# Performance work log

Hardware: AMD Instinct MI355X
Metric: run time of the kernel (lower is better)

The kernel has to match this reference:

```python
import jax, jax.numpy as jnp
import numpy as np

N, E, D, DE, H = 50000, 400000, 128, 64, 8
EPS = 1e-5
SLOPE = 0.2


def setup_inputs() -> dict:
    key = jax.random.key(0)
    ks = jax.random.split(key, 16)

    def lin(k, fan_in, fan_out):
        return (jax.random.normal(k, (fan_in, fan_out), jnp.float32) / np.sqrt(fan_in)).astype(jnp.float32)

    return {
        "node_features": jax.random.normal(ks[0], (N, D), jnp.float32),
        "edge_features": jax.random.normal(ks[1], (E, DE), jnp.float32),
        "Wn": lin(ks[2], D, D), "bn": jnp.zeros((D,), jnp.float32),
        "Wq": lin(ks[3], D, D), "bq": jnp.zeros((D,), jnp.float32),
        "Wk": lin(ks[4], D, D), "bk": jnp.zeros((D,), jnp.float32),
        "Wv": lin(ks[5], D, D), "bv": jnp.zeros((D,), jnp.float32),
        "We": lin(ks[6], DE, D), "be": jnp.zeros((D,), jnp.float32),
        "A1": lin(ks[7], 3 * D, D), "b1": jnp.zeros((D,), jnp.float32),
        "A2": lin(ks[8], D, H), "b2": jnp.zeros((H,), jnp.float32),
        "gamma": jnp.ones((D,), jnp.float32),
        "beta": jnp.zeros((D,), jnp.float32),
        "edge_index": jax.random.randint(ks[9], (2, E), 0, N, dtype=jnp.int32),
    }


def reference(node_features, edge_features, Wn, bn, Wq, bq, Wk, bk, Wv, bv,
              We, be, A1, b1, A2, b2, gamma, beta, edge_index):
    num_nodes = node_features.shape[0]
    h = node_features @ Wn + bn                      # [N, D]
    q = node_features @ Wq + bq                      # [N, D]
    k = node_features @ Wk + bk                      # [N, D]
    v = node_features @ Wv + bv                      # [N, D]
    eh = edge_features @ We + be                     # [E, D]

    src, tgt = edge_index[0], edge_index[1]
    attn_in = jnp.concatenate([q[src], k[tgt], eh], axis=-1)   # [E, 3D]
    hmid = jax.nn.leaky_relu(attn_in @ A1 + b1, SLOPE)          # [E, D]
    scores = jax.nn.leaky_relu(hmid @ A2 + b2, SLOPE)           # [E, H]
    w = jax.nn.softmax(scores.mean(axis=-1), axis=0)            # global softmax over edges, [E]

    # scatter-add: output[src] += w * v[tgt]
    out = jax.ops.segment_sum(w[:, None] * v[tgt], src, num_segments=num_nodes)  # [N, D]

    y = h + out                                       # dropout = identity (eval)
    mu = y.mean(axis=-1, keepdims=True)
    var = y.var(axis=-1, keepdims=True)
    return gamma * (y - mu) / jnp.sqrt(var + EPS) + beta
```

## Files before the change

### kernel.cpp

```cpp
#include <hip/hip_runtime.h>

#define D 128
#define DE 64
#define SLOPE 0.2f
#define EPS 1e-5f

typedef float f32x4 __attribute__((ext_vector_type(4)));
typedef short bf16x8 __attribute__((ext_vector_type(8)));
typedef unsigned short ushort;

__device__ __forceinline__ float lrelu(float x) { return x > 0.f ? x : SLOPE * x; }

__device__ __forceinline__ ushort f2bf(float x) {
  union { float f; unsigned u; } c; c.f = x;
  unsigned r = c.u + 0x7FFFu + ((c.u >> 16) & 1u);
  return (ushort)(r >> 16);
}
__device__ __forceinline__ float bf2f(unsigned u) {
  return __uint_as_float(u << 16);
}
__device__ __forceinline__ uint4 cvt8(const float* p) {
  float4 f0 = *(const float4*)p;
  float4 f1 = *(const float4*)(p + 4);
  union { ushort us[8]; uint4 v; } u;
  u.us[0] = f2bf(f0.x); u.us[1] = f2bf(f0.y);
  u.us[2] = f2bf(f0.z); u.us[3] = f2bf(f0.w);
  u.us[4] = f2bf(f1.x); u.us[5] = f2bf(f1.y);
  u.us[6] = f2bf(f1.z); u.us[7] = f2bf(f1.w);
  return u.v;
}

__global__ __launch_bounds__(128) void fold_pack(
    const float* __restrict__ Wq, const float* __restrict__ Wk,
    const float* __restrict__ We, const float* __restrict__ A1,
    const float* __restrict__ bq, const float* __restrict__ bk,
    const float* __restrict__ be, const float* __restrict__ b1,
    const float* __restrict__ Wn, const float* __restrict__ Wv,
    ushort* __restrict__ AfqP, ushort* __restrict__ AfkP,
    ushort* __restrict__ AfeT, float* __restrict__ bfold,
    ushort* __restrict__ WnP, ushort* __restrict__ WvP,
    const int* __restrict__ src, int* __restrict__ deg, int E) {
  int r = blockIdx.x;
  int j = threadIdx.x;
  if (r < 128) {
    float acc = 0.f;
    for (int t = 0; t < 128; ++t) acc += Wq[r * 128 + t] * A1[t * 128 + j];
    int ch = r >> 5, quad = (r >> 3) & 3, jj = r & 7, nt = j >> 4, l15 = j & 15;
    AfqP[(((ch * 8 + nt) * 4 + quad) * 16 + l15) * 8 + jj] = f2bf(acc);
  } else if (r < 256) {
    int k = r - 128;
    float acc = 0.f;
    for (int t = 0; t < 128; ++t) acc += Wk[k * 128 + t] * A1[(128 + t) * 128 + j];
    int ch = k >> 5, quad = (k >> 3) & 3, jj = k & 7, nt = j >> 4, l15 = j & 15;
    AfkP[(((ch * 8 + nt) * 4 + quad) * 16 + l15) * 8 + jj] = f2bf(acc);
  } else if (r < 320) {
    int k = r - 256;
    float acc = 0.f;
    for (int t = 0; t < 128; ++t) acc += We[k * 128 + t] * A1[(256 + t) * 128 + j];
    AfeT[j * 64 + k] = f2bf(acc);
  } else if (r == 320) {
    float acc = b1[j];
    for (int t = 0; t < 128; ++t) {
      acc += bq[t] * A1[t * 128 + j];
      acc += bk[t] * A1[(128 + t) * 128 + j];
      acc += be[t] * A1[(256 + t) * 128 + j];
    }
    bfold[j] = acc;
  } else if (r < 449) {
    int c = r - 321;
    int ch = j >> 5, quad = (j >> 3) & 3, jj = j & 7, nt = c >> 4, l15 = c & 15;
    WnP[(((ch * 8 + nt) * 4 + quad) * 16 + l15) * 8 + jj] = f2bf(Wn[j * 128 + c]);
  } else if (r < 577) {
    int c = r - 449;
    int ch = j >> 5, quad = (j >> 3) & 3, jj = j & 7, nt = c >> 4, l15 = c & 15;
    WvP[(((ch * 8 + nt) * 4 + quad) * 16 + l15) * 8 + jj] = f2bf(Wv[j * 128 + c]);
  } else {
    int i = (r - 577) * 128 + j;
    if (i < E) atomicAdd(&deg[src[i]], 1);
  }
}

__global__ __launch_bounds__(256, 2) void node_gemm_mfma(
    const float* __restrict__ X, const ushort* __restrict__ WnP,
    const ushort* __restrict__ WvP, const ushort* __restrict__ AfqP,
    const ushort* __restrict__ AfkP, const float* __restrict__ bn,
    const float* __restrict__ bv, float* __restrict__ h,
    ushort* __restrict__ vb, ushort* __restrict__ q2p,
    ushort* __restrict__ k2p, int Nn) {
  __shared__ ushort As[128 * 40];
  __shared__ float bS[128];
  const ushort* BP;
  const float* bb = nullptr;
  float* O = nullptr;
  ushort* Ob = nullptr;
  int mode;
  switch (blockIdx.y) {
    case 0: BP = WnP; bb = bn; O = h; mode = 0; break;
    case 1: BP = WvP; bb = bv; Ob = vb; mode = 1; break;
    case 2: BP = AfqP; Ob = q2p; mode = 2; break;
    default: BP = AfkP; Ob = k2p; mode = 2; break;
  }
  const int t = threadIdx.x;
  if (t < 128) bS[t] = bb ? bb[t] : 0.f;
  const int seg = t & 3, arow = t >> 2;
  const int m0 = blockIdx.x * 128;
  int rIdx[2];
#pragma unroll
  for (int l = 0; l < 2; ++l) rIdx[l] = min(m0 + arow + 64 * l, Nn - 1);
  uint4 avA[2];
#pragma unroll
  for (int l = 0; l < 2; ++l)
    avA[l] = cvt8(X + (size_t)rIdx[l] * 128 + seg * 8);
  f32x4 acc[2][8];
#pragma unroll
  for (int mt = 0; mt < 2; ++mt)
#pragma unroll
    for (int nt = 0; nt < 8; ++nt) acc[mt][nt] = (f32x4)(0.f);
  const int lane = t & 63, wv = t >> 6, l15 = lane & 15, quad = lane >> 4;
  for (int ch = 0; ch < 4; ++ch) {
#pragma unroll
    for (int l = 0; l < 2; ++l)
      *(uint4*)&As[(arow + 64 * l) * 40 + seg * 8] = avA[l];
    __syncthreads();
    if (ch < 3) {
      int o = (ch + 1) * 32 + seg * 8;
#pragma unroll
      for (int l = 0; l < 2; ++l)
        avA[l] = cvt8(X + (size_t)rIdx[l] * 128 + o);
    }
    bf16x8 af[2];
#pragma unroll
    for (int mt = 0; mt < 2; ++mt)
      af[mt] = *(const bf16x8*)&As[(wv * 32 + mt * 16 + l15) * 40 + quad * 8];
    const ushort* bp = BP + ((size_t)(ch * 8) * 64 + lane) * 8;
#pragma unroll
    for (int nt = 0; nt < 8; ++nt) {
      bf16x8 bfr = *(const bf16x8*)(bp + nt * 512);
#pragma unroll
      for (int mt = 0; mt < 2; ++mt)
        acc[mt][nt] =
            __builtin_amdgcn_mfma_f32_16x16x32_bf16(af[mt], bfr, acc[mt][nt], 0, 0, 0);
    }
    __syncthreads();
  }
#pragma unroll
  for (int mt = 0; mt < 2; ++mt) {
    int rowb = m0 + wv * 32 + mt * 16 + quad * 4;
#pragma unroll
    for (int nt = 0; nt < 8; ++nt) {
      int col = nt * 16 + l15;
      float b = bS[col];
#pragma unroll
      for (int r = 0; r < 4; ++r) {
        int rg = rowb + r;
        if (rg < Nn) {
          if (mode == 0)      O[(size_t)rg * 128 + col] = acc[mt][nt][r] + b;
          else if (mode == 1) Ob[(size_t)rg * 128 + col] = f2bf(acc[mt][nt][r] + b);
          else                Ob[(size_t)rg * 128 + l15 * 8 + nt] = f2bf(acc[mt][nt][r]);
        }
      }
    }
  }
}

__global__ __launch_bounds__(256, 3) void edge_fused4(
    const float* __restrict__ EF, const ushort* __restrict__ AfeT,
    const float* __restrict__ bfold, const float* __restrict__ A2,
    const float* __restrict__ b2, const ushort* __restrict__ q2p,
    const ushort* __restrict__ k2p, const int* __restrict__ src,
    const int* __restrict__ tgt, int* __restrict__ cursor,
    int2* __restrict__ cwt, float2* __restrict__ part, int E) {
  __shared__ ushort As[128 * 40];
  __shared__ ushort Bs[128 * 40];
  __shared__ float A2s[128 * 9];
  __shared__ float bfS[128];
  __shared__ float b2s[8];
  __shared__ int sIdxS[128], sIdxT[128];
  __shared__ float redM[16], redS[16];
  const int t = threadIdx.x;
  const int e0 = blockIdx.x * 128;
  if (t < 128) {
    sIdxS[t] = src[min(e0 + t, E - 1)];
    bfS[t] = bfold[t];
  } else {
    sIdxT[t - 128] = tgt[min(e0 + t - 128, E - 1)];
  }
  if (t < 8) b2s[t] = b2[t];
#pragma unroll
  for (int l = 0; l < 4; ++l) {
    int i = t + l * 256;
    A2s[(i >> 3) * 9 + (i & 7)] = A2[i];
  }
  const int seg = t & 3, arow = t >> 2;
  int ecl[2];
#pragma unroll
  for (int l = 0; l < 2; ++l) ecl[l] = min(e0 + arow + 64 * l, E - 1);
  uint4 avA[2], avB[2];
#pragma unroll
  for (int l = 0; l < 2; ++l) {
    avA[l] = cvt8(EF + (size_t)ecl[l] * 64 + seg * 8);
    avB[l] = *(const uint4*)(AfeT + (arow + 64 * l) * 64 + seg * 8);
  }
  f32x4 acc[2][8];
#pragma unroll
  for (int mt = 0; mt < 2; ++mt)
#pragma unroll
    for (int nt = 0; nt < 8; ++nt) acc[mt][nt] = (f32x4)(0.f);
  const int lane = t & 63, wv = t >> 6, l15 = lane & 15, quad = lane >> 4;

#pragma unroll
  for (int ch = 0; ch < 2; ++ch) {
#pragma unroll
    for (int l = 0; l < 2; ++l) {
      *(uint4*)&As[(arow + 64 * l) * 40 + seg * 8] = avA[l];
      *(uint4*)&Bs[(arow + 64 * l) * 40 + seg * 8] = avB[l];
    }
    __syncthreads();
    if (ch == 0) {
      int o = 32 + seg * 8;
#pragma unroll
      for (int l = 0; l < 2; ++l) {
        avA[l] = cvt8(EF + (size_t)ecl[l] * 64 + o);
        avB[l] = *(const uint4*)(AfeT + (arow + 64 * l) * 64 + o);
      }
    }
    bf16x8 af[2];
#pragma unroll
    for (int mt = 0; mt < 2; ++mt)
      af[mt] = *(const bf16x8*)&As[(wv * 32 + mt * 16 + l15) * 40 + quad * 8];
#pragma unroll
    for (int nt = 0; nt < 8; ++nt) {
      bf16x8 bfr = *(const bf16x8*)&Bs[(nt * 16 + l15) * 40 + quad * 8];
#pragma unroll
      for (int mt = 0; mt < 2; ++mt)
        acc[mt][nt] =
            __builtin_amdgcn_mfma_f32_16x16x32_bf16(af[mt], bfr, acc[mt][nt], 0, 0, 0);
    }
    if (ch == 0) __syncthreads();
  }

  float bfv[8];
#pragma unroll
  for (int nt = 0; nt < 8; ++nt) bfv[nt] = bfS[nt * 16 + l15];
#pragma unroll
  for (int mt = 0; mt < 2; ++mt) {
#pragma unroll
    for (int r = 0; r < 4; ++r) {
      int erow = wv * 32 + mt * 16 + quad * 4 + r;
      int si = sIdxS[erow], ti = sIdxT[erow];
      uint4 qv = *(const uint4*)(q2p + (size_t)si * 128 + l15 * 8);
      uint4 kv = *(const uint4*)(k2p + (size_t)ti * 128 + l15 * 8);
      const ushort* qs = (const ushort*)&qv;
      const ushort* ks = (const ushort*)&kv;
#pragma unroll
      for (int nt = 0; nt < 8; ++nt)
        acc[mt][nt][r] =
            lrelu(acc[mt][nt][r] + bf2f(qs[nt]) + bf2f(ks[nt]) + bfv[nt]);
    }
  }
  float tacc[2][4];
#pragma unroll
  for (int mt = 0; mt < 2; ++mt)
#pragma unroll
    for (int r = 0; r < 4; ++r) tacc[mt][r] = 0.f;
  for (int hh = 0; hh < 8; ++hh) {
    float a2v[8];
#pragma unroll
    for (int nt = 0; nt < 8; ++nt) a2v[nt] = A2s[nt * 144 + l15 * 9 + hh];
    float b2h = b2s[hh];
#pragma unroll
    for (int mt = 0; mt < 2; ++mt)
#pragma unroll
      for (int r = 0; r < 4; ++r) {
        float p = 0.f;
#pragma unroll
        for (int nt = 0; nt < 8; ++nt) p += acc[mt][nt][r] * a2v[nt];
        p += __shfl_xor(p, 1);
        p += __shfl_xor(p, 2);
        p += __shfl_xor(p, 4);
        p += __shfl_xor(p, 8);
        tacc[mt][r] += lrelu(p + b2h);
      }
  }
  if (l15 == 0) {
    float sc[8];
    float m = -1e30f;
#pragma unroll
    for (int mt = 0; mt < 2; ++mt)
#pragma unroll
      for (int r = 0; r < 4; ++r) {
        int i = mt * 4 + r;
        sc[i] = tacc[mt][r] * 0.125f;
        int e = e0 + wv * 32 + mt * 16 + quad * 4 + r;
        if (e < E) m = fmaxf(m, sc[i]);
      }
    float ssum = 0.f;
#pragma unroll
    for (int mt = 0; mt < 2; ++mt)
#pragma unroll
      for (int r = 0; r < 4; ++r) {
        int i = mt * 4 + r;
        int erow = wv * 32 + mt * 16 + quad * 4 + r;
        if (e0 + erow < E) {
          ssum += __expf(sc[i] - m);
          int j = atomicAdd(&cursor[sIdxS[erow]], 1);
          cwt[j] = make_int2(sIdxT[erow], __float_as_int(sc[i]));
        }
      }
    int rid = wv * 4 + quad;
    redM[rid] = m;
    redS[rid] = ssum;
  }
  __syncthreads();
  if (t == 0) {
    float M = redM[0], S = redS[0];
#pragma unroll
    for (int i = 1; i < 16; ++i) {
      float m2 = redM[i], s2 = redS[i];
      float Mn = fmaxf(M, m2);
      S = S * __expf(M - Mn) + s2 * __expf(m2 - Mn);
      M = Mn;
    }
    part[blockIdx.x] = make_float2(M, S);
  }
}

__global__ __launch_bounds__(256) void softmax_final(
    const float2* __restrict__ part, int nPart, float* __restrict__ MS) {
  __shared__ float mS[256], sS[256];
  int tid = threadIdx.x;
  float m = -1e30f, sum = 0.f;
  for (int i = tid; i < nPart; i += 256) {
    float2 p = part[i];
    float M = fmaxf(m, p.x);
    sum = sum * __expf(m - M) + p.y * __expf(p.x - M);
    m = M;
  }
  mS[tid] = m;
  sS[tid] = sum;
  __syncthreads();
  for (int off = 128; off > 0; off >>= 1) {
    if (tid < off) {
      float m1 = mS[tid], s1 = sS[tid];
      float m2 = mS[tid + off], s2 = sS[tid + off];
      float M = fmaxf(m1, m2);
      mS[tid] = M;
      sS[tid] = s1 * __expf(m1 - M) + s2 * __expf(m2 - M);
    }
    __syncthreads();
  }
  if (tid == 0) {
    MS[0] = mS[0];
    MS[1] = 1.f / sS[0];
  }
}

__global__ __launch_bounds__(256) void scan1(const int* __restrict__ deg,
                                             int* __restrict__ incl,
                                             int* __restrict__ bsum, int N) {
  __shared__ int sh[256];
  int tid = threadIdx.x;
  int i = blockIdx.x * 256 + tid;
  sh[tid] = (i < N) ? deg[i] : 0;
  __syncthreads();
  for (int off = 1; off < 256; off <<= 1) {
    int tv = (tid >= off) ? sh[tid - off] : 0;
    __syncthreads();
    sh[tid] += tv;
    __syncthreads();
  }
  if (i < N) incl[i] = sh[tid];
  if (tid == 255) bsum[blockIdx.x] = sh[255];
}

__global__ __launch_bounds__(256) void scan2(int* __restrict__ bsum, int nb) {
  __shared__ int sh[256];
  int tid = threadIdx.x;
  sh[tid] = (tid < nb) ? bsum[tid] : 0;
  __syncthreads();
  for (int off = 1; off < 256; off <<= 1) {
    int tv = (tid >= off) ? sh[tid - off] : 0;
    __syncthreads();
    sh[tid] += tv;
    __syncthreads();
  }
  if (tid < nb) bsum[tid] = sh[tid];
}

__global__ __launch_bounds__(256) void scan3(const int* __restrict__ deg,
                                             const int* __restrict__ incl,
                                             const int* __restrict__ bsum,
                                             int* __restrict__ offs,
                                             int* __restrict__ cursor, int N,
                                             int E) {
  int i = blockIdx.x * 256 + threadIdx.x;
  if (i >= N) return;
  int base = (blockIdx.x > 0) ? bsum[blockIdx.x - 1] : 0;
  int ex = incl[i] - deg[i] + base;
  offs[i] = ex;
  cursor[i] = ex;
  if (i == N - 1) offs[N] = E;
}

__global__ __launch_bounds__(256) void gather_ln(
    const int* __restrict__ offs, const int2* __restrict__ cwt,
    const ushort* __restrict__ vb, const float* __restrict__ MS,
    const float* __restrict__ gamma, const float* __restrict__ beta,
    float* __restrict__ y, int N) {
  int tid = threadIdx.x;
  int n = blockIdx.x * 4 + (tid >> 6);
  if (n >= N) return;
  int lane = tid & 63;
  float M = MS[0], inv = MS[1];
  int beg = offs[n], end = offs[n + 1];
  float a0 = 0.f, a1 = 0.f;
  int j = beg;
  for (; j + 4 <= end; j += 4) {
    int2 p0 = cwt[j], p1 = cwt[j + 1], p2 = cwt[j + 2], p3 = cwt[j + 3];
    unsigned u0 = *(const unsigned*)(vb + (size_t)p0.x * 128 + lane * 2);
    unsigned u1 = *(const unsigned*)(vb + (size_t)p1.x * 128 + lane * 2);
    unsigned u2 = *(const unsigned*)(vb + (size_t)p2.x * 128 + lane * 2);
    unsigned u3 = *(const unsigned*)(vb + (size_t)p3.x * 128 + lane * 2);
    float w0 = __expf(__int_as_float(p0.y) - M) * inv;
    float w1 = __expf(__int_as_float(p1.y) - M) * inv;
    float w2 = __expf(__int_as_float(p2.y) - M) * inv;
    float w3 = __expf(__int_as_float(p3.y) - M) * inv;
    a0 += w0 * bf2f(u0 & 0xffffu) + w1 * bf2f(u1 & 0xffffu) +
          w2 * bf2f(u2 & 0xffffu) + w3 * bf2f(u3 & 0xffffu);
    a1 += w0 * bf2f(u0 >> 16) + w1 * bf2f(u1 >> 16) + w2 * bf2f(u2 >> 16) +
          w3 * bf2f(u3 >> 16);
  }
  for (; j < end; ++j) {
    int2 p = cwt[j];
    float w = __expf(__int_as_float(p.y) - M) * inv;
    unsigned u = *(const unsigned*)(vb + (size_t)p.x * 128 + lane * 2);
    a0 += w * bf2f(u & 0xffffu);
    a1 += w * bf2f(u >> 16);
  }
  size_t base = (size_t)n * 128 + lane * 2;
  float2 hv = *(const float2*)(y + base);
  float y0 = hv.x + a0, y1 = hv.y + a1;
  float sum = y0 + y1, ssq = y0 * y0 + y1 * y1;
#pragma unroll
  for (int off = 1; off < 64; off <<= 1) {
    sum += __shfl_xor(sum, off);
    ssq += __shfl_xor(ssq, off);
  }
  float mu = sum * (1.f / 128.f);
  float var = ssq * (1.f / 128.f) - mu * mu;
  float rstd = rsqrtf(var + EPS);
  float2 g = *(const float2*)(gamma + lane * 2);
  float2 bt = *(const float2*)(beta + lane * 2);
  float2 out;
  out.x = g.x * (y0 - mu) * rstd + bt.x;
  out.y = g.y * (y1 - mu) * rstd + bt.y;
  *(float2*)(y + base) = out;
}

extern "C" void kernel_launch(void* const* d_in, const int* in_sizes, int n_in,
                              void* d_out, int out_size, void* d_ws,
                              size_t ws_size, hipStream_t stream) {
  const float* X  = (const float*)d_in[0];
  const float* EF = (const float*)d_in[1];
  const float* Wn = (const float*)d_in[2];
  const float* bn = (const float*)d_in[3];
  const float* Wq = (const float*)d_in[4];
  const float* bq = (const float*)d_in[5];
  const float* Wk = (const float*)d_in[6];
  const float* bk = (const float*)d_in[7];
  const float* Wv = (const float*)d_in[8];
  const float* bv = (const float*)d_in[9];
  const float* We = (const float*)d_in[10];
  const float* be = (const float*)d_in[11];
  const float* A1 = (const float*)d_in[12];
  const float* b1 = (const float*)d_in[13];
  const float* A2 = (const float*)d_in[14];
  const float* b2 = (const float*)d_in[15];
  const float* gamma = (const float*)d_in[16];
  const float* beta  = (const float*)d_in[17];
  const int* ei = (const int*)d_in[18];

  int N = in_sizes[0] / D;
  int E = in_sizes[1] / DE;
  const int* src = ei;
  const int* tgt = ei + E;

  float* h = (float*)d_out;
  float* ws = (float*)d_ws;
  float2* part = (float2*)ws;
  float* MS    = (float*)(part + 4096);
  float* bfold = MS + 4;
  ushort* vb   = (ushort*)(bfold + 128);
  ushort* q2p  = vb + (size_t)N * D;
  ushort* k2p  = q2p + (size_t)N * D;
  ushort* AfqP = k2p + (size_t)N * D;
  ushort* AfkP = AfqP + 128 * 128;
  ushort* AfeT = AfkP + 128 * 128;
  ushort* WnP  = AfeT + 128 * 64;
  ushort* WvP  = WnP + 128 * 128;
  int* deg    = (int*)(WvP + 128 * 128);
  int* incl   = deg + N;
  int* bsum   = incl + N;
  int* cursor = bsum + 256;
  int* offs   = cursor + N;
  int2* cwt   = (int2*)(offs + N + 2);

  int nbScan = (N + 255) / 256;
  int nbEdge = (E + 127) / 128;
  int nbHist = (E + 127) / 128;

  hipMemsetAsync(deg, 0, (size_t)N * sizeof(int), stream);
  fold_pack<<<577 + nbHist, 128, 0, stream>>>(Wq, Wk, We, A1, bq, bk, be, b1,
                                              Wn, Wv, AfqP, AfkP, AfeT, bfold,
                                              WnP, WvP, src, deg, E);
  scan1<<<nbScan, 256, 0, stream>>>(deg, incl, bsum, N);
  scan2<<<1, 256, 0, stream>>>(bsum, nbScan);
  scan3<<<nbScan, 256, 0, stream>>>(deg, incl, bsum, offs, cursor, N, E);
  node_gemm_mfma<<<dim3((N + 127) / 128, 4), 256, 0, stream>>>(
      X, WnP, WvP, AfqP, AfkP, bn, bv, h, vb, q2p, k2p, N);
  edge_fused4<<<nbEdge, 256, 0, stream>>>(EF, AfeT, bfold, A2, b2, q2p, k2p,
                                          src, tgt, cursor, cwt, part, E);
  softmax_final<<<1, 256, 0, stream>>>(part, nbEdge, MS);
  gather_ln<<<(N + 3) / 4, 256, 0, stream>>>(offs, cwt, vb, MS, gamma, beta, h,
                                             N);
}
```

Measured before the change: 381.1 us.

## Fuse four node GEMMs into one kernel sharing a staged input tile

The node GEMM previously ran four grid slices (Wn, Wv, folded q, folded k), each reloading and converting the same 128-row block of node features from global memory. Now each block stages its full 128x128 bf16 input tile into shared memory once and loops over the four weight sets, reusing the tile. This cuts X reads and conversions fourfold. In exchange the grid has a quarter as many blocks, shared memory per block grows to about 35 KB, and the chunked prefetch overlap of the old loop is gone.

```diff
diff --git a/kernel.cpp b/kernel.cpp
--- a/kernel.cpp
+++ b/kernel.cpp
@@ -80,83 +80,81 @@
   }
 }
 
-__global__ __launch_bounds__(256, 2) void node_gemm_mfma(
+__global__ __launch_bounds__(256, 2) void node_gemm_fused(
     const float* __restrict__ X, const ushort* __restrict__ WnP,
     const ushort* __restrict__ WvP, const ushort* __restrict__ AfqP,
     const ushort* __restrict__ AfkP, const float* __restrict__ bn,
     const float* __restrict__ bv, float* __restrict__ h,
     ushort* __restrict__ vb, ushort* __restrict__ q2p,
     ushort* __restrict__ k2p, int Nn) {
-  __shared__ ushort As[128 * 40];
-  __shared__ float bS[128];
-  const ushort* BP;
-  const float* bb = nullptr;
-  float* O = nullptr;
-  ushort* Ob = nullptr;
-  int mode;
-  switch (blockIdx.y) {
-    case 0: BP = WnP; bb = bn; O = h; mode = 0; break;
-    case 1: BP = WvP; bb = bv; Ob = vb; mode = 1; break;
-    case 2: BP = AfqP; Ob = q2p; mode = 2; break;
-    default: BP = AfkP; Ob = k2p; mode = 2; break;
-  }
+  __shared__ ushort As[128 * 136];
+  __shared__ float bnS[128], bvS[128];
   const int t = threadIdx.x;
-  if (t < 128) bS[t] = bb ? bb[t] : 0.f;
-  const int seg = t & 3, arow = t >> 2;
+  if (t < 128) {
+    bnS[t] = bn[t];
+    bvS[t] = bv[t];
+  }
   const int m0 = blockIdx.x * 128;
-  int rIdx[2];
-#pragma unroll
-  for (int l = 0; l < 2; ++l) rIdx[l] = min(m0 + arow + 64 * l, Nn - 1);
-  uint4 avA[2];
-#pragma unroll
-  for (int l = 0; l < 2; ++l)
-    avA[l] = cvt8(X + (size_t)rIdx[l] * 128 + seg * 8);
-  f32x4 acc[2][8];
-#pragma unroll
-  for (int mt = 0; mt < 2; ++mt)
-#pragma unroll
-    for (int nt = 0; nt < 8; ++nt) acc[mt][nt] = (f32x4)(0.f);
+  {
+    int row = t >> 1, half = t & 1;
+    int rg = min(m0 + row, Nn - 1);
+    const float* xp = X + (size_t)rg * 128 + half * 64;
+    ushort* ap = &As[row * 136 + half * 64];
+#pragma unroll
+    for (int s = 0; s < 8; ++s) *(uint4*)(ap + s * 8) = cvt8(xp + s * 8);
+  }
+  __syncthreads();
   const int lane = t & 63, wv = t >> 6, l15 = lane & 15, quad = lane >> 4;
-  for (int ch = 0; ch < 4; ++ch) {
-#pragma unroll
-    for (int l = 0; l < 2; ++l)
-      *(uint4*)&As[(arow + 64 * l) * 40 + seg * 8] = avA[l];
-    __syncthreads();
-    if (ch < 3) {
-      int o = (ch + 1) * 32 + seg * 8;
-#pragma unroll
-      for (int l = 0; l < 2; ++l)
-        avA[l] = cvt8(X + (size_t)rIdx[l] * 128 + o);
-    }
-    bf16x8 af[2];
+#pragma unroll 1
+  for (int mode = 0; mode < 4; ++mode) {
+    const ushort* BP;
+    switch (mode) {
+      case 0: BP = WnP; break;
+      case 1: BP = WvP; break;
+      case 2: BP = AfqP; break;
+      default: BP = AfkP; break;
+    }
+    f32x4 acc[2][8];
 #pragma unroll
     for (int mt = 0; mt < 2; ++mt)
-      af[mt] = *(const bf16x8*)&As[(wv * 32 + mt * 16 + l15) * 40 + quad * 8];
-    const ushort* bp = BP + ((size_t)(ch * 8) * 64 + lane) * 8;
-#pragma unroll
-    for (int nt = 0; nt < 8; ++nt) {
-      bf16x8 bfr = *(const bf16x8*)(bp + nt * 512);
+#pragma unroll
+      for (int nt = 0; nt < 8; ++nt) acc[mt][nt] = (f32x4)(0.f);
+#pragma unroll
+    for (int ch = 0; ch < 4; ++ch) {
+      bf16x8 af[2];
 #pragma unroll
       for (int mt = 0; mt < 2; ++mt)
-        acc[mt][nt] =
-            __builtin_amdgcn_mfma_f32_16x16x32_bf16(af[mt], bfr, acc[mt][nt], 0, 0, 0);
-    }
-    __syncthreads();
-  }
-#pragma unroll
-  for (int mt = 0; mt < 2; ++mt) {
-    int rowb = m0 + wv * 32 + mt * 16 + quad * 4;
-#pragma unroll
-    for (int nt = 0; nt < 8; ++nt) {
-      int col = nt * 16 + l15;
-      float b = bS[col];
-#pragma unroll
-      for (int r = 0; r < 4; ++r) {
-        int rg = rowb + r;
-        if (rg < Nn) {
-          if (mode == 0)      O[(size_t)rg * 128 + col] = acc[mt][nt][r] + b;
-          else if (mode == 1) Ob[(size_t)rg * 128 + col] = f2bf(acc[mt][nt][r] + b);
-          else                Ob[(size_t)rg * 128 + l15 * 8 + nt] = f2bf(acc[mt][nt][r]);
+        af[mt] = *(const bf16x8*)&As[(wv * 32 + mt * 16 + l15) * 136 +
+                                     ch * 32 + quad * 8];
+      const ushort* bp = BP + ((size_t)(ch * 8) * 64 + lane) * 8;
+#pragma unroll
+      for (int nt = 0; nt < 8; ++nt) {
+        bf16x8 bfr = *(const bf16x8*)(bp + nt * 512);
+#pragma unroll
+        for (int mt = 0; mt < 2; ++mt)
+          acc[mt][nt] = __builtin_amdgcn_mfma_f32_16x16x32_bf16(
+              af[mt], bfr, acc[mt][nt], 0, 0, 0);
+      }
+    }
+#pragma unroll
+    for (int mt = 0; mt < 2; ++mt) {
+      int rowb = m0 + wv * 32 + mt * 16 + quad * 4;
+#pragma unroll
+      for (int nt = 0; nt < 8; ++nt) {
+        int col = nt * 16 + l15;
+#pragma unroll
+        for (int r = 0; r < 4; ++r) {
+          int rg = rowb + r;
+          if (rg < Nn) {
+            if (mode == 0)
+              h[(size_t)rg * 128 + col] = acc[mt][nt][r] + bnS[col];
+            else if (mode == 1)
+              vb[(size_t)rg * 128 + col] = f2bf(acc[mt][nt][r] + bvS[col]);
+            else if (mode == 2)
+              q2p[(size_t)rg * 128 + l15 * 8 + nt] = f2bf(acc[mt][nt][r]);
+            else
+              k2p[(size_t)rg * 128 + l15 * 8 + nt] = f2bf(acc[mt][nt][r]);
+          }
         }
       }
     }
@@ -516,7 +514,7 @@
   scan1<<<nbScan, 256, 0, stream>>>(deg, incl, bsum, N);
   scan2<<<1, 256, 0, stream>>>(bsum, nbScan);
   scan3<<<nbScan, 256, 0, stream>>>(deg, incl, bsum, offs, cursor, N, E);
-  node_gemm_mfma<<<dim3((N + 127) / 128, 4), 256, 0, stream>>>(
+  node_gemm_fused<<<(N + 127) / 128, 256, 0, stream>>>(
       X, WnP, WvP, AfqP, AfkP, bn, bv, h, vb, q2p, k2p, N);
   edge_fused4<<<nbEdge, 256, 0, stream>>>(EF, AfeT, bfold, A2, b2, q2p, k2p,
                                           src, tgt, cursor, cwt, part, E);
```

Result: slower. 396.5 us (+4.0%).
